# Performance work log

Measured on AMD Instinct MI355X. Metric: run time of the kernel, lower is better.

Reference implementation:

```python
import jax, jax.numpy as jnp
import numpy as np
import math

D_MODEL = 2048
D_QK = 128
D_V = 128
SEQ = 4096

def setup_inputs() -> dict:
    key = jax.random.key(0)
    ks = jax.random.split(key, 9)
    s = 1.0 / math.sqrt(D_MODEL)
    return {
        "input_q": jax.random.normal(ks[0], (SEQ, D_MODEL), jnp.float32),
        "input_k": jax.random.normal(ks[1], (SEQ, D_MODEL), jnp.float32),
        "input_v": jax.random.normal(ks[2], (SEQ, D_MODEL), jnp.float32),
        "WQ_w": jax.random.normal(ks[3], (D_QK, D_MODEL), jnp.float32) * s,
        "WQ_b": jax.random.normal(ks[4], (D_QK,), jnp.float32) * s,
        "WK_w": jax.random.normal(ks[5], (D_QK, D_MODEL), jnp.float32) * s,
        "WK_b": jax.random.normal(ks[6], (D_QK,), jnp.float32) * s,
        "WV_w": jax.random.normal(ks[7], (D_V, D_MODEL), jnp.float32) * s,
        "WV_b": jax.random.normal(ks[8], (D_V,), jnp.float32) * s,
    }

def reference(input_q, input_k, input_v, WQ_w, WQ_b, WK_w, WK_b, WV_w, WV_b):
    # Linear projections (torch nn.Linear: x @ W.T + b)
    Q = input_q @ WQ_w.T + WQ_b   # [S, d_qk]
    K = input_k @ WK_w.T + WK_b   # [S, d_qk]
    V = input_v @ WV_w.T + WV_b   # [S, d_v]
    S = Q.shape[0]
    # causal mask: -inf strictly above the diagonal, 0 elsewhere
    mask = jnp.triu(jnp.full((S, S), -jnp.inf, dtype=Q.dtype), k=1)
    # NOTE: original code adds mask BEFORE dividing by sqrt(d_model)
    scores = (Q @ K.T + mask) / math.sqrt(D_MODEL)  # [S, S]
    attn = jax.nn.softmax(scores, axis=-1)
    return attn @ V  # [S, d_v]
```

## Files before the change

### kernel.cpp

```cpp
#include <hip/hip_runtime.h>

#define SEQ 4096
#define DM  2048
#define DH  128
#define NSPLIT 8

typedef __attribute__((ext_vector_type(8))) short bf16x8;
typedef __attribute__((ext_vector_type(4))) short short4v;
typedef __attribute__((ext_vector_type(4))) float f32x4;

__device__ inline short f2bf(float f) {
    union { float f; unsigned u; } x; x.f = f;
    unsigned r = x.u + 0x7fffu + ((x.u >> 16) & 1u);
    return (short)(r >> 16);
}

__device__ inline float fexp2(float f) { return __builtin_amdgcn_exp2f(f); }

__device__ inline void lds_barrier() {
    asm volatile("s_waitcnt lgkmcnt(0)\n\ts_barrier" ::: "memory");
}

__global__ __launch_bounds__(256) void convw_kernel(
    const float* __restrict__ wq, const float* __restrict__ wk, const float* __restrict__ wv,
    short* __restrict__ Wbf)
{
    int idx = blockIdx.x * 256 + threadIdx.x;
    int mat = idx >> 16;
    int off = (idx & 65535) * 4;
    const float* W = (mat == 0) ? wq : (mat == 1) ? wk : wv;
    float4 v = *reinterpret_cast<const float4*>(W + off);
    short4v s = { f2bf(v.x), f2bf(v.y), f2bf(v.z), f2bf(v.w) };
    *reinterpret_cast<short4v*>(Wbf + (size_t)mat * DH * DM + off) = s;
}

__global__ __launch_bounds__(256) void proj_kernel(
    const float* __restrict__ inq, const float* __restrict__ ink, const float* __restrict__ inv,
    const short* __restrict__ Wbf,
    float* __restrict__ Pqk, float* __restrict__ Pv)
{
    const int mat = blockIdx.y;
    const int s   = blockIdx.z;
    const float* A = (mat == 0) ? inq : (mat == 1) ? ink : inv;

    const int tid  = threadIdx.x;
    const int lane = tid & 63;
    const int w    = tid >> 6;
    const int g    = lane >> 4;
    const int c16  = lane & 15;
    const int i0   = blockIdx.x * 64;
    const int kb   = s * 512;

    __shared__ short Alds[64][72];
    __shared__ short Wlds[128][72];

    const int ar = tid >> 2, ac = (tid & 3) * 16;
    const float* Aload = A + (size_t)(i0 + ar) * DM + kb + ac;
    const int wr = tid >> 1, wc = (tid & 1) * 32;
    const short* Wload = Wbf + (size_t)mat * DH * DM + (size_t)wr * DM + kb + wc;

    f32x4 acc[2][4];
    #pragma unroll
    for (int mI = 0; mI < 2; mI++)
        #pragma unroll
        for (int n = 0; n < 4; n++) acc[mI][n] = (f32x4){0.f, 0.f, 0.f, 0.f};

    float4  abuf[4][4];
    bf16x8  wbuf[2][4];

    #pragma unroll
    for (int d = 0; d < 2; d++) {
        #pragma unroll
        for (int j = 0; j < 4; j++)
            wbuf[d][j] = *reinterpret_cast<const bf16x8*>(Wload + d * 64 + j * 8);
        #pragma unroll
        for (int j = 0; j < 4; j++)
            abuf[d][j] = *reinterpret_cast<const float4*>(Aload + d * 64 + j * 4);
    }
    #pragma unroll
    for (int d = 2; d < 4; d++)
        #pragma unroll
        for (int j = 0; j < 4; j++)
            abuf[d][j] = *reinterpret_cast<const float4*>(Aload + d * 64 + j * 4);

    const int rw = (w >> 1) * 32;
    const int cw = (w & 1) * 64;

    #pragma unroll
    for (int c = 0; c < 8; c++) {
        const int da = c & 3, dw = c & 1;
        {
            #pragma unroll
            for (int j = 0; j < 4; j++)
                *reinterpret_cast<bf16x8*>(&Wlds[wr][wc + j * 8]) = wbuf[dw][j];
            #pragma unroll
            for (int j = 0; j < 2; j++) {
                float4 v0 = abuf[da][j * 2], v1 = abuf[da][j * 2 + 1];
                bf16x8 sv = { f2bf(v0.x), f2bf(v0.y), f2bf(v0.z), f2bf(v0.w),
                              f2bf(v1.x), f2bf(v1.y), f2bf(v1.z), f2bf(v1.w) };
                *reinterpret_cast<bf16x8*>(&Alds[ar][ac + j * 8]) = sv;
            }
        }
        if (c + 2 < 8) {
            #pragma unroll
            for (int j = 0; j < 4; j++)
                wbuf[dw][j] = *reinterpret_cast<const bf16x8*>(Wload + (c + 2) * 64 + j * 8);
        }
        if (c + 4 < 8) {
            #pragma unroll
            for (int j = 0; j < 4; j++)
                abuf[da][j] = *reinterpret_cast<const float4*>(Aload + (c + 4) * 64 + j * 4);
        }
        lds_barrier();
        #pragma unroll
        for (int kk = 0; kk < 2; kk++) {
            bf16x8 af0 = *reinterpret_cast<const bf16x8*>(&Alds[rw + c16][kk * 32 + g * 8]);
            bf16x8 af1 = *reinterpret_cast<const bf16x8*>(&Alds[rw + 16 + c16][kk * 32 + g * 8]);
            #pragma unroll
            for (int n = 0; n < 4; n++) {
                bf16x8 wf = *reinterpret_cast<const bf16x8*>(
                    &Wlds[cw + n * 16 + c16][kk * 32 + g * 8]);
                acc[0][n] = __builtin_amdgcn_mfma_f32_16x16x32_bf16(af0, wf, acc[0][n], 0, 0, 0);
                acc[1][n] = __builtin_amdgcn_mfma_f32_16x16x32_bf16(af1, wf, acc[1][n], 0, 0, 0);
            }
        }
        lds_barrier();
    }

    if (mat < 2) {
        float* outp = Pqk + ((size_t)(mat * 4 + s) * SEQ) * DH;
        #pragma unroll
        for (int mI = 0; mI < 2; mI++) {
            int row0 = i0 + rw + mI * 16 + g * 4;
            #pragma unroll
            for (int n = 0; n < 4; n++) {
                int col = cw + n * 16 + c16;
                #pragma unroll
                for (int r = 0; r < 4; r++)
                    outp[(size_t)(row0 + r) * DH + col] = acc[mI][n][r];
            }
        }
    } else {
        float* outp = Pv + (size_t)s * DH * SEQ;
        #pragma unroll
        for (int mI = 0; mI < 2; mI++) {
            int row0 = i0 + rw + mI * 16 + g * 4;
            #pragma unroll
            for (int n = 0; n < 4; n++) {
                int col = cw + n * 16 + c16;
                float4 f = { acc[mI][n][0], acc[mI][n][1], acc[mI][n][2], acc[mI][n][3] };
                *reinterpret_cast<float4*>(&outp[(size_t)col * SEQ + row0]) = f;
            }
        }
    }
}

__global__ __launch_bounds__(256) void combine_kernel(
    const float* __restrict__ Pqk, const float* __restrict__ Pv,
    const float* __restrict__ bq, const float* __restrict__ bk, const float* __restrict__ bv,
    short* __restrict__ Qws, short* __restrict__ Kws, short* __restrict__ Vtws)
{
    const int b = blockIdx.x;
    if (b < 1024) {
        int tid = b * 256 + threadIdx.x;
        int mat = tid >> 17;
        int idx4 = (tid & 131071) * 4;
        float4 acc = {0.f, 0.f, 0.f, 0.f};
        #pragma unroll
        for (int s = 0; s < 4; s++) {
            float4 p = *reinterpret_cast<const float4*>(
                Pqk + ((size_t)(mat * 4 + s) * SEQ) * DH + idx4);
            acc.x += p.x; acc.y += p.y; acc.z += p.z; acc.w += p.w;
        }
        const float* bias = (mat == 0) ? bq : bk;
        int col = idx4 & (DH - 1);
        acc.x += bias[col]; acc.y += bias[col + 1]; acc.z += bias[col + 2]; acc.w += bias[col + 3];
        short4v o = { f2bf(acc.x), f2bf(acc.y), f2bf(acc.z), f2bf(acc.w) };
        short* outp = (mat == 0) ? Qws : Kws;
        *reinterpret_cast<short4v*>(outp + idx4) = o;
    } else {
        int tid = (b - 1024) * 256 + threadIdx.x;
        int idx4 = tid * 4;
        float4 acc = {0.f, 0.f, 0.f, 0.f};
        #pragma unroll
        for (int s = 0; s < 4; s++) {
            float4 p = *reinterpret_cast<const float4*>(Pv + (size_t)s * DH * SEQ + idx4);
            acc.x += p.x; acc.y += p.y; acc.z += p.z; acc.w += p.w;
        }
        float bvv = bv[idx4 >> 12];
        acc.x += bvv; acc.y += bvv; acc.z += bvv; acc.w += bvv;
        short4v o = { f2bf(acc.x), f2bf(acc.y), f2bf(acc.z), f2bf(acc.w) };
        *reinterpret_cast<short4v*>(Vtws + idx4) = o;
    }
}

__global__ __launch_bounds__(256) void flash_kernel(
    const short* __restrict__ Qws, const short* __restrict__ Kws, const short* __restrict__ Vtws,
    float* __restrict__ Opart, float* __restrict__ mpart, float* __restrict__ lpart)
{
    const int qb = blockIdx.x;
    const int y  = blockIdx.y;
    const int tid = threadIdx.x;
    const int w    = tid >> 6;
    const int lane = tid & 63;
    const int g = lane >> 4, c16 = lane & 15;
    const int i0 = qb * 64 + w * 16;

    __shared__ short Klds[64][136];
    __shared__ short Vlds[128][72];
    __shared__ short Slds[4][16][72];

    const int kkey = tid >> 2,  kdim = (tid & 3) * 32;
    const int vdim = tid >> 1,  vkey = (tid & 1) * 32;

    bf16x8 kreg[4], vreg[4];

    bf16x8 qf[4];
    #pragma unroll
    for (int kk = 0; kk < 4; kk++)
        qf[kk] = *reinterpret_cast<const bf16x8*>(Qws + (size_t)(i0 + c16) * DH + kk * 32 + g * 8);

    float m[4], lsum[4];
    f32x4 O[8];
    #pragma unroll
    for (int r = 0; r < 4; r++) { m[r] = -__builtin_inff(); lsum[r] = 0.f; }
    #pragma unroll
    for (int c = 0; c < 8; c++) O[c] = (f32x4){0.f, 0.f, 0.f, 0.f};

    const float C = 0.03188448666f;

    if (qb >= y) {
        {
            const int j0 = y * 64;
            #pragma unroll
            for (int j = 0; j < 4; j++) {
                kreg[j] = *reinterpret_cast<const bf16x8*>(
                    Kws + (size_t)(j0 + kkey) * DH + kdim + j * 8);
                vreg[j] = *reinterpret_cast<const bf16x8*>(
                    Vtws + (size_t)vdim * SEQ + j0 + vkey + j * 8);
            }
            #pragma unroll
            for (int j = 0; j < 4; j++) {
                *reinterpret_cast<bf16x8*>(&Klds[kkey][kdim + j * 8]) = kreg[j];
                *reinterpret_cast<bf16x8*>(&Vlds[vdim][vkey + j * 8]) = vreg[j];
            }
        }
        lds_barrier();

        for (int jt = y; jt <= qb; jt += NSPLIT) {
            const bool more = (jt + NSPLIT <= qb);
            if (more) {
                const int jn = (jt + NSPLIT) * 64;
                #pragma unroll
                for (int j = 0; j < 4; j++) {
                    kreg[j] = *reinterpret_cast<const bf16x8*>(
                        Kws + (size_t)(jn + kkey) * DH + kdim + j * 8);
                    vreg[j] = *reinterpret_cast<const bf16x8*>(
                        Vtws + (size_t)vdim * SEQ + jn + vkey + j * 8);
                }
            }
            const int j0 = jt * 64;
            f32x4 S[4];
            #pragma unroll
            for (int t = 0; t < 4; t++) S[t] = (f32x4){0.f, 0.f, 0.f, 0.f};
            #pragma unroll
            for (int kk = 0; kk < 4; kk++) {
                #pragma unroll
                for (int t = 0; t < 4; t++) {
                    bf16x8 kf = *reinterpret_cast<const bf16x8*>(
                        &Klds[t * 16 + c16][kk * 32 + g * 8]);
                    S[t] = __builtin_amdgcn_mfma_f32_16x16x32_bf16(qf[kk], kf, S[t], 0, 0, 0);
                }
            }
            float s2[4][4];
            #pragma unroll
            for (int t = 0; t < 4; t++) {
                int key = j0 + t * 16 + c16;
                #pragma unroll
                for (int r = 0; r < 4; r++) {
                    int q = i0 + g * 4 + r;
                    s2[t][r] = (key > q) ? -__builtin_inff() : S[t][r] * C;
                }
            }
            float mnew[4], alpha[4];
            #pragma unroll
            for (int r = 0; r < 4; r++) {
                float rm = fmaxf(fmaxf(s2[0][r], s2[1][r]), fmaxf(s2[2][r], s2[3][r]));
                rm = fmaxf(rm, __shfl_xor(rm, 1));
                rm = fmaxf(rm, __shfl_xor(rm, 2));
                rm = fmaxf(rm, __shfl_xor(rm, 4));
                rm = fmaxf(rm, __shfl_xor(rm, 8));
                mnew[r] = fmaxf(m[r], rm);
                alpha[r] = fexp2(m[r] - mnew[r]);
                m[r] = mnew[r];
            }
            #pragma unroll
            for (int r = 0; r < 4; r++) {
                float ps = 0.f;
                #pragma unroll
                for (int t = 0; t < 4; t++) {
                    float p = fexp2(s2[t][r] - mnew[r]);
                    ps += p;
                    Slds[w][g * 4 + r][t * 16 + c16] = f2bf(p);
                }
                ps += __shfl_xor(ps, 1);
                ps += __shfl_xor(ps, 2);
                ps += __shfl_xor(ps, 4);
                ps += __shfl_xor(ps, 8);
                lsum[r] = lsum[r] * alpha[r] + ps;
                #pragma unroll
                for (int c = 0; c < 8; c++) O[c][r] *= alpha[r];
            }
            #pragma unroll
            for (int kk2 = 0; kk2 < 2; kk2++) {
                bf16x8 pf = *reinterpret_cast<const bf16x8*>(&Slds[w][c16][kk2 * 32 + g * 8]);
                #pragma unroll
                for (int c = 0; c < 8; c++) {
                    bf16x8 vf = *reinterpret_cast<const bf16x8*>(
                        &Vlds[c * 16 + c16][kk2 * 32 + g * 8]);
                    O[c] = __builtin_amdgcn_mfma_f32_16x16x32_bf16(pf, vf, O[c], 0, 0, 0);
                }
            }
            lds_barrier();
            if (more) {
                #pragma unroll
                for (int j = 0; j < 4; j++) {
                    *reinterpret_cast<bf16x8*>(&Klds[kkey][kdim + j * 8]) = kreg[j];
                    *reinterpret_cast<bf16x8*>(&Vlds[vdim][vkey + j * 8]) = vreg[j];
                }
                lds_barrier();
            }
        }
        #pragma unroll
        for (int c = 0; c < 8; c++) {
            int col = c * 16 + c16;
            #pragma unroll
            for (int r = 0; r < 4; r++)
                Opart[((size_t)y * SEQ + i0 + g * 4 + r) * DH + col] = O[c][r];
        }
    }
    if (c16 == 0) {
        #pragma unroll
        for (int r = 0; r < 4; r++) {
            mpart[y * SEQ + i0 + g * 4 + r] = m[r];
            lpart[y * SEQ + i0 + g * 4 + r] = lsum[r];
        }
    }
}

__global__ __launch_bounds__(256) void merge_kernel(
    const float* __restrict__ Opart, const float* __restrict__ mpart, const float* __restrict__ lpart,
    float* __restrict__ out, int NS)
{
    const int row = blockIdx.x * 2 + (threadIdx.x >> 7);
    const int col = threadIdx.x & 127;
    float mh[16];
    float M = -__builtin_inff();
    for (int hh = 0; hh < NS; hh++) {
        mh[hh] = mpart[hh * SEQ + row];
        M = fmaxf(M, mh[hh]);
    }
    float denom = 0.f, num = 0.f;
    for (int hh = 0; hh < NS; hh++) {
        float wgt = fexp2(mh[hh] - M);
        denom += lpart[hh * SEQ + row] * wgt;
        num   += Opart[((size_t)hh * SEQ + row) * DH + col] * wgt;
    }
    out[(size_t)row * DH + col] = num / denom;
}

extern "C" void kernel_launch(void* const* d_in, const int* in_sizes, int n_in,
                              void* d_out, int out_size, void* d_ws, size_t ws_size,
                              hipStream_t stream) {
    const float* inq = (const float*)d_in[0];
    const float* ink = (const float*)d_in[1];
    const float* inv = (const float*)d_in[2];
    const float* wq  = (const float*)d_in[3];
    const float* bq  = (const float*)d_in[4];
    const float* wk  = (const float*)d_in[5];
    const float* bk  = (const float*)d_in[6];
    const float* wv  = (const float*)d_in[7];
    const float* bv  = (const float*)d_in[8];

    char* ws = (char*)d_ws;
    short* Qws   = (short*)(ws);
    short* Kws   = (short*)(ws + (1u << 20));
    short* Vtws  = (short*)(ws + (2u << 20));
    short* Wbf   = (short*)(ws + (3u << 20));
    float* Pqk   = (float*)(ws + 4718592);
    float* Pv    = (float*)(ws + 21495808);
    float* Opart = (float*)(ws + (3u << 20));
    float* mpart = (float*)(ws + (3u << 20) + (size_t)NSPLIT * SEQ * DH * 4);
    float* lpart = mpart + (size_t)NSPLIT * SEQ;

    convw_kernel<<<768, 256, 0, stream>>>(wq, wk, wv, Wbf);
    proj_kernel<<<dim3(64, 3, 4), 256, 0, stream>>>(inq, ink, inv, Wbf, Pqk, Pv);
    combine_kernel<<<1536, 256, 0, stream>>>(Pqk, Pv, bq, bk, bv, Qws, Kws, Vtws);
    flash_kernel<<<dim3(64, NSPLIT), 256, 0, stream>>>(Qws, Kws, Vtws, Opart, mpart, lpart);
    merge_kernel<<<2048, 256, 0, stream>>>(Opart, mpart, lpart, (float*)d_out, NSPLIT);
}
```

Measured before the change: 182.1 us.

## Drop split-K in projection and fuse bias/bf16 conversion, removing combine kernel

The projection kernel now processes the full 2048-wide reduction per block with 32-row tiles instead of four K-splits writing fp32 partials. Bias addition and bf16 conversion move into its epilogue, so the separate combine kernel and its partial-sum global traffic are removed. This trades fewer blocks and a longer serial loop per block for less memory traffic and one fewer launch.

```diff
diff --git a/kernel.cpp b/kernel.cpp
--- a/kernel.cpp
+++ b/kernel.cpp
@@ -37,89 +37,79 @@
 __global__ __launch_bounds__(256) void proj_kernel(
     const float* __restrict__ inq, const float* __restrict__ ink, const float* __restrict__ inv,
     const short* __restrict__ Wbf,
-    float* __restrict__ Pqk, float* __restrict__ Pv)
+    const float* __restrict__ bq, const float* __restrict__ bk, const float* __restrict__ bv,
+    short* __restrict__ Qws, short* __restrict__ Kws, short* __restrict__ Vtws)
 {
     const int mat = blockIdx.y;
-    const int s   = blockIdx.z;
-    const float* A = (mat == 0) ? inq : (mat == 1) ? ink : inv;
+    const float* A    = (mat == 0) ? inq : (mat == 1) ? ink : inv;
+    const float* bias = (mat == 0) ? bq  : (mat == 1) ? bk  : bv;
 
     const int tid  = threadIdx.x;
     const int lane = tid & 63;
     const int w    = tid >> 6;
     const int g    = lane >> 4;
     const int c16  = lane & 15;
-    const int i0   = blockIdx.x * 64;
-    const int kb   = s * 512;
-
-    __shared__ short Alds[64][72];
+    const int i0   = blockIdx.x * 32;
+
+    __shared__ short Alds[32][72];
     __shared__ short Wlds[128][72];
 
-    const int ar = tid >> 2, ac = (tid & 3) * 16;
-    const float* Aload = A + (size_t)(i0 + ar) * DM + kb + ac;
+    const int ar = tid >> 3, ac = (tid & 7) * 8;
+    const float* Aload = A + (size_t)(i0 + ar) * DM + ac;
     const int wr = tid >> 1, wc = (tid & 1) * 32;
-    const short* Wload = Wbf + (size_t)mat * DH * DM + (size_t)wr * DM + kb + wc;
-
-    f32x4 acc[2][4];
+    const short* Wload = Wbf + (size_t)mat * DH * DM + (size_t)wr * DM + wc;
+
+    f32x4 acc[2][2];
     #pragma unroll
     for (int mI = 0; mI < 2; mI++)
         #pragma unroll
-        for (int n = 0; n < 4; n++) acc[mI][n] = (f32x4){0.f, 0.f, 0.f, 0.f};
-
-    float4  abuf[4][4];
+        for (int n = 0; n < 2; n++) acc[mI][n] = (f32x4){0.f, 0.f, 0.f, 0.f};
+
+    float4  abuf[4][2];
     bf16x8  wbuf[2][4];
 
     #pragma unroll
-    for (int d = 0; d < 2; d++) {
+    for (int d = 0; d < 2; d++)
         #pragma unroll
         for (int j = 0; j < 4; j++)
             wbuf[d][j] = *reinterpret_cast<const bf16x8*>(Wload + d * 64 + j * 8);
-        #pragma unroll
-        for (int j = 0; j < 4; j++)
+    #pragma unroll
+    for (int d = 0; d < 4; d++)
+        #pragma unroll
+        for (int j = 0; j < 2; j++)
             abuf[d][j] = *reinterpret_cast<const float4*>(Aload + d * 64 + j * 4);
-    }
-    #pragma unroll
-    for (int d = 2; d < 4; d++)
-        #pragma unroll
-        for (int j = 0; j < 4; j++)
-            abuf[d][j] = *reinterpret_cast<const float4*>(Aload + d * 64 + j * 4);
-
-    const int rw = (w >> 1) * 32;
-    const int cw = (w & 1) * 64;
-
-    #pragma unroll
-    for (int c = 0; c < 8; c++) {
+
+    #pragma unroll
+    for (int c = 0; c < 32; c++) {
         const int da = c & 3, dw = c & 1;
         {
             #pragma unroll
             for (int j = 0; j < 4; j++)
                 *reinterpret_cast<bf16x8*>(&Wlds[wr][wc + j * 8]) = wbuf[dw][j];
-            #pragma unroll
-            for (int j = 0; j < 2; j++) {
-                float4 v0 = abuf[da][j * 2], v1 = abuf[da][j * 2 + 1];
-                bf16x8 sv = { f2bf(v0.x), f2bf(v0.y), f2bf(v0.z), f2bf(v0.w),
-                              f2bf(v1.x), f2bf(v1.y), f2bf(v1.z), f2bf(v1.w) };
-                *reinterpret_cast<bf16x8*>(&Alds[ar][ac + j * 8]) = sv;
-            }
-        }
-        if (c + 2 < 8) {
+            float4 v0 = abuf[da][0], v1 = abuf[da][1];
+            bf16x8 sv = { f2bf(v0.x), f2bf(v0.y), f2bf(v0.z), f2bf(v0.w),
+                          f2bf(v1.x), f2bf(v1.y), f2bf(v1.z), f2bf(v1.w) };
+            *reinterpret_cast<bf16x8*>(&Alds[ar][ac]) = sv;
+        }
+        if (c + 2 < 32) {
             #pragma unroll
             for (int j = 0; j < 4; j++)
                 wbuf[dw][j] = *reinterpret_cast<const bf16x8*>(Wload + (c + 2) * 64 + j * 8);
         }
-        if (c + 4 < 8) {
-            #pragma unroll
-            for (int j = 0; j < 4; j++)
+        if (c + 4 < 32) {
+            #pragma unroll
+            for (int j = 0; j < 2; j++)
                 abuf[da][j] = *reinterpret_cast<const float4*>(Aload + (c + 4) * 64 + j * 4);
         }
         lds_barrier();
         #pragma unroll
         for (int kk = 0; kk < 2; kk++) {
-            bf16x8 af0 = *reinterpret_cast<const bf16x8*>(&Alds[rw + c16][kk * 32 + g * 8]);
-            bf16x8 af1 = *reinterpret_cast<const bf16x8*>(&Alds[rw + 16 + c16][kk * 32 + g * 8]);
-            #pragma unroll
-            for (int n = 0; n < 4; n++) {
+            bf16x8 af0 = *reinterpret_cast<const bf16x8*>(&Alds[c16][kk * 32 + g * 8]);
+            bf16x8 af1 = *reinterpret_cast<const bf16x8*>(&Alds[16 + c16][kk * 32 + g * 8]);
+            #pragma unroll
+            for (int n = 0; n < 2; n++) {
                 bf16x8 wf = *reinterpret_cast<const bf16x8*>(
-                    &Wlds[cw + n * 16 + c16][kk * 32 + g * 8]);
+                    &Wlds[w * 32 + n * 16 + c16][kk * 32 + g * 8]);
                 acc[0][n] = __builtin_amdgcn_mfma_f32_16x16x32_bf16(af0, wf, acc[0][n], 0, 0, 0);
                 acc[1][n] = __builtin_amdgcn_mfma_f32_16x16x32_bf16(af1, wf, acc[1][n], 0, 0, 0);
             }
@@ -128,69 +118,32 @@
     }
 
     if (mat < 2) {
-        float* outp = Pqk + ((size_t)(mat * 4 + s) * SEQ) * DH;
+        short* outp = (mat == 0) ? Qws : Kws;
         #pragma unroll
         for (int mI = 0; mI < 2; mI++) {
-            int row0 = i0 + rw + mI * 16 + g * 4;
-            #pragma unroll
-            for (int n = 0; n < 4; n++) {
-                int col = cw + n * 16 + c16;
+            int row0 = i0 + mI * 16 + g * 4;
+            #pragma unroll
+            for (int n = 0; n < 2; n++) {
+                int col = w * 32 + n * 16 + c16;
+                float b = bias[col];
                 #pragma unroll
                 for (int r = 0; r < 4; r++)
-                    outp[(size_t)(row0 + r) * DH + col] = acc[mI][n][r];
+                    outp[(size_t)(row0 + r) * DH + col] = f2bf(acc[mI][n][r] + b);
             }
         }
     } else {
-        float* outp = Pv + (size_t)s * DH * SEQ;
         #pragma unroll
         for (int mI = 0; mI < 2; mI++) {
-            int row0 = i0 + rw + mI * 16 + g * 4;
-            #pragma unroll
-            for (int n = 0; n < 4; n++) {
-                int col = cw + n * 16 + c16;
-                float4 f = { acc[mI][n][0], acc[mI][n][1], acc[mI][n][2], acc[mI][n][3] };
-                *reinterpret_cast<float4*>(&outp[(size_t)col * SEQ + row0]) = f;
-            }
-        }
-    }
-}
-
-__global__ __launch_bounds__(256) void combine_kernel(
-    const float* __restrict__ Pqk, const float* __restrict__ Pv,
-    const float* __restrict__ bq, const float* __restrict__ bk, const float* __restrict__ bv,
-    short* __restrict__ Qws, short* __restrict__ Kws, short* __restrict__ Vtws)
-{
-    const int b = blockIdx.x;
-    if (b < 1024) {
-        int tid = b * 256 + threadIdx.x;
-        int mat = tid >> 17;
-        int idx4 = (tid & 131071) * 4;
-        float4 acc = {0.f, 0.f, 0.f, 0.f};
-        #pragma unroll
-        for (int s = 0; s < 4; s++) {
-            float4 p = *reinterpret_cast<const float4*>(
-                Pqk + ((size_t)(mat * 4 + s) * SEQ) * DH + idx4);
-            acc.x += p.x; acc.y += p.y; acc.z += p.z; acc.w += p.w;
-        }
-        const float* bias = (mat == 0) ? bq : bk;
-        int col = idx4 & (DH - 1);
-        acc.x += bias[col]; acc.y += bias[col + 1]; acc.z += bias[col + 2]; acc.w += bias[col + 3];
-        short4v o = { f2bf(acc.x), f2bf(acc.y), f2bf(acc.z), f2bf(acc.w) };
-        short* outp = (mat == 0) ? Qws : Kws;
-        *reinterpret_cast<short4v*>(outp + idx4) = o;
-    } else {
-        int tid = (b - 1024) * 256 + threadIdx.x;
-        int idx4 = tid * 4;
-        float4 acc = {0.f, 0.f, 0.f, 0.f};
-        #pragma unroll
-        for (int s = 0; s < 4; s++) {
-            float4 p = *reinterpret_cast<const float4*>(Pv + (size_t)s * DH * SEQ + idx4);
-            acc.x += p.x; acc.y += p.y; acc.z += p.z; acc.w += p.w;
-        }
-        float bvv = bv[idx4 >> 12];
-        acc.x += bvv; acc.y += bvv; acc.z += bvv; acc.w += bvv;
-        short4v o = { f2bf(acc.x), f2bf(acc.y), f2bf(acc.z), f2bf(acc.w) };
-        *reinterpret_cast<short4v*>(Vtws + idx4) = o;
+            int row0 = i0 + mI * 16 + g * 4;
+            #pragma unroll
+            for (int n = 0; n < 2; n++) {
+                int col = w * 32 + n * 16 + c16;
+                float b = bias[col];
+                short4v o = { f2bf(acc[mI][n][0] + b), f2bf(acc[mI][n][1] + b),
+                              f2bf(acc[mI][n][2] + b), f2bf(acc[mI][n][3] + b) };
+                *reinterpret_cast<short4v*>(Vtws + (size_t)col * SEQ + row0) = o;
+            }
+        }
     }
 }
 
@@ -387,15 +340,12 @@
     short* Kws   = (short*)(ws + (1u << 20));
     short* Vtws  = (short*)(ws + (2u << 20));
     short* Wbf   = (short*)(ws + (3u << 20));
-    float* Pqk   = (float*)(ws + 4718592);
-    float* Pv    = (float*)(ws + 21495808);
-    float* Opart = (float*)(ws + (3u << 20));
-    float* mpart = (float*)(ws + (3u << 20) + (size_t)NSPLIT * SEQ * DH * 4);
+    float* Opart = (float*)(ws + 4718592);
+    float* mpart = (float*)(ws + 4718592 + (size_t)NSPLIT * SEQ * DH * 4);
     float* lpart = mpart + (size_t)NSPLIT * SEQ;
 
     convw_kernel<<<768, 256, 0, stream>>>(wq, wk, wv, Wbf);
-    proj_kernel<<<dim3(64, 3, 4), 256, 0, stream>>>(inq, ink, inv, Wbf, Pqk, Pv);
-    combine_kernel<<<1536, 256, 0, stream>>>(Pqk, Pv, bq, bk, bv, Qws, Kws, Vtws);
+    proj_kernel<<<dim3(128, 3), 256, 0, stream>>>(inq, ink, inv, Wbf, bq, bk, bv, Qws, Kws, Vtws);
     flash_kernel<<<dim3(64, NSPLIT), 256, 0, stream>>>(Qws, Kws, Vtws, Opart, mpart, lpart);
     merge_kernel<<<2048, 256, 0, stream>>>(Opart, mpart, lpart, (float*)d_out, NSPLIT);
 }
```

After: 189.2 us. 3.9% more time.
